# Optimization experiments

Hardware: AMD Instinct MI355X
Metric: run time of the kernel (lower is better)

Reference implementation:

```python
import jax, jax.numpy as jnp
import numpy as np

EPS = 1e-6


def _clinear(xr, xi, wr, wi):
    # nn.Linear applies x @ W.T; complex multiply (xr+i*xi)(Wr+i*Wi)
    r = xr @ wr.T - xi @ wi.T
    im = xi @ wr.T + xr @ wi.T
    return r, im


def setup_inputs() -> dict:
    key = jax.random.key(0)
    ks = jax.random.split(key, 11)
    B, S, D = 16384, 16, 64
    return {
        "z_real": jax.random.normal(ks[0], (B, D), jnp.float32),
        "z_imag": jax.random.normal(ks[1], (B, D), jnp.float32),
        "mem": jax.random.normal(ks[2], (B, S, 2 * D), jnp.float32),
        "ptr": jax.random.uniform(ks[3], (B, S), jnp.float32),
        "ctrl": jax.random.normal(ks[4], (B, 3), jnp.float32),
        "w_q_real": jax.random.normal(ks[5], (D, D), jnp.float32),
        "w_q_imag": jax.random.normal(ks[6], (D, D), jnp.float32),
        "w_k_real": jax.random.normal(ks[7], (D, D), jnp.float32),
        "w_k_imag": jax.random.normal(ks[8], (D, D), jnp.float32),
        "w_v_real": jax.random.normal(ks[9], (D, D), jnp.float32),
        "w_v_imag": jax.random.normal(ks[10], (D, D), jnp.float32),
    }


def reference(z_real, z_imag, mem, ptr, ctrl,
              w_q_real, w_q_imag, w_k_real, w_k_imag, w_v_real, w_v_imag):
    D = z_real.shape[-1]
    scale = D ** (-0.5)

    # differentiable push/pop/stay gates
    g = jax.nn.sigmoid(ctrl)                      # [B, 3]
    total = g.sum(-1, keepdims=True) + EPS
    push = (g[:, 0:1] / total)                    # [B, 1]
    pop = (g[:, 1:2] / total)
    stay = (g[:, 2:3] / total)

    # pointer shifts (torch.roll semantics)
    ptr_up = jnp.roll(ptr, 1, axis=1)
    ptr_down = jnp.roll(ptr, -1, axis=1)
    new_ptr = push * ptr_up + pop * ptr_down + stay * ptr  # [B, S]

    # blended write of current state into every memory slot
    z_flat = jnp.concatenate([z_real, z_imag], axis=-1)    # [B, 2D]
    p = push[:, :, None]                                   # [B, 1, 1]
    mem_new = mem * (1.0 - p) + p * z_flat[:, None, :]     # [B, S, 2D]

    mr, mi = mem_new[..., :D], mem_new[..., D:]

    # complex attention over memory slots
    qr, qi = _clinear(mr, mi, w_q_real, w_q_imag)
    kr, ki = _clinear(mr, mi, w_k_real, w_k_imag)
    vr, vi = _clinear(mr, mi, w_v_real, w_v_imag)
    q_flat = jnp.concatenate([qr, qi], axis=-1)            # [B, S, 2D]
    k_flat = jnp.concatenate([kr, ki], axis=-1)
    scores = jnp.einsum('bsd,btd->bst', q_flat, k_flat) * scale
    attn = jax.nn.softmax(scores, axis=-1)                 # [B, S, S]
    ar = jnp.einsum('bst,btd->bsd', attn, vr)
    ai = jnp.einsum('bst,btd->bsd', attn, vi)
    attended_flat = jnp.concatenate([ar, ai], axis=-1)     # [B, S, 2D]

    # pointer-weighted read
    read_flat = (attended_flat * new_ptr[:, :, None]).sum(1)  # [B, 2D]
    z_read_real = read_flat[:, :D]
    z_read_imag = read_flat[:, D:]

    active_slots = (new_ptr > 0.1).astype(jnp.float32).sum(1).mean()
    return z_read_real, z_read_imag, mem_new, new_ptr, active_slots
```

## Files before the change

kernel.cpp:

```cpp
#include <hip/hip_runtime.h>
#include <math.h>

#define GRID  256
#define BLK   512
#define NB    8
#define NITER 8

typedef __attribute__((ext_vector_type(8))) short short8;
typedef __attribute__((ext_vector_type(4))) float f32x4;

__device__ __forceinline__ float sigf(float x) { return 1.0f / (1.0f + expf(-x)); }

__device__ __forceinline__ unsigned short f2bf(float x) {
    unsigned u = __float_as_uint(x);
    return (unsigned short)((u + 0x7fffu + ((u >> 16) & 1u)) >> 16);
}
__device__ __forceinline__ float bf2f(unsigned short h) {
    return __uint_as_float(((unsigned)h) << 16);
}

__device__ __forceinline__ void split8(const float4 p0, const float4 p1,
                                       short8& hi, short8& lo) {
    float xs[8] = {p0.x, p0.y, p0.z, p0.w, p1.x, p1.y, p1.z, p1.w};
#pragma unroll
    for (int i = 0; i < 8; ++i) {
        unsigned short h = f2bf(xs[i]);
        hi[i] = (short)h;
        lo[i] = (short)f2bf(xs[i] - bf2f(h));
    }
}

__device__ __forceinline__ float Mmat(const float* __restrict__ wr,
                                      const float* __restrict__ wi, int k, int j) {
    if (j < 64) return (k < 64) ? wr[j * 64 + k] : -wi[j * 64 + (k - 64)];
    return (k < 64) ? wi[(j - 64) * 64 + k] : wr[(j - 64) * 64 + (k - 64)];
}

__global__ void prep_kernel(const float* __restrict__ wqr, const float* __restrict__ wqi,
                            const float* __restrict__ wkr, const float* __restrict__ wki,
                            const float* __restrict__ wvr, const float* __restrict__ wvi,
                            float* __restrict__ G, float* __restrict__ Mv,
                            int* __restrict__ cnt) {
    const int a = blockIdx.x;
    const int bb = threadIdx.x;
    if (a == 0 && bb == 0) *cnt = 0;
    float acc = 0.f;
    for (int j = 0; j < 128; ++j)
        acc += Mmat(wqr, wqi, a, j) * Mmat(wkr, wki, bb, j);
    G[a * 128 + bb] = 0.125f * acc;
    Mv[a * 128 + bb] = Mmat(wvr, wvi, a, bb);
}

__global__ void prep_frag(const float* __restrict__ G, const float* __restrict__ Mv,
                          unsigned short* __restrict__ Gf, unsigned short* __restrict__ Mvf) {
    const int bid = blockIdx.x;
    const int lane = threadIdx.x;
    const int mat = bid >> 5, jt = (bid >> 2) & 7, t = bid & 3;
    const float* X = mat ? Mv : G;
    unsigned short* O = mat ? Mvf : Gf;
    const int quad = lane >> 4, col = lane & 15;
    const int obase = ((jt * 4 + t) * 2) * 512 + lane * 8;
#pragma unroll
    for (int i = 0; i < 8; ++i) {
        int k = t * 32 + quad * 8 + i;
        int j = jt * 16 + col;
        float x = X[k * 128 + j];
        unsigned short h = f2bf(x);
        O[obase + i] = h;
        O[obase + 512 + i] = f2bf(x - bf2f(h));
    }
}

__global__ __launch_bounds__(BLK, 2) void crsn_main(
    const float* __restrict__ z_real, const float* __restrict__ z_imag,
    const float* __restrict__ mem, const float* __restrict__ ptr,
    const float* __restrict__ ctrl,
    const unsigned short* __restrict__ Gf, const unsigned short* __restrict__ Mvf,
    float* __restrict__ o_zr, float* __restrict__ o_zi,
    float* __restrict__ o_mem, float* __restrict__ o_np,
    int* __restrict__ g_cnt) {
    __shared__ __align__(16) float buf[16896];
    __shared__ __align__(16) unsigned short mfrag[33280];
    __shared__ float npl[NB][16];
    __shared__ float wl[NB][16];
    __shared__ float pushl[NB], popl[NB], stayl[NB];
    __shared__ int cnt_lds;

    const int tid = threadIdx.x;
    const int w = tid >> 6;
    const int lane = tid & 63;
    const int quad = lane >> 4;
    const int col = lane & 15;

    if (tid == 0) cnt_lds = 0;

    f32x4 acc1[NB], acc2[NB];

    for (int it = 0; it < NITER; ++it) {
        const int base = blockIdx.x * (NB * NITER) + it * NB;

        if (tid < NB) {
            int b = base + tid;
            float g0 = sigf(ctrl[b * 3 + 0]);
            float g1 = sigf(ctrl[b * 3 + 1]);
            float g2 = sigf(ctrl[b * 3 + 2]);
            float tot = g0 + g1 + g2 + 1e-6f;
            pushl[tid] = g0 / tot; popl[tid] = g1 / tot; stayl[tid] = g2 / tot;
        }

        {
            const float* gsrc = mem + (size_t)base * 2048 + w * 2048;
#pragma unroll
            for (int c = 0; c < 8; ++c) {
                __builtin_amdgcn_global_load_lds(
                    (const __attribute__((address_space(1))) unsigned int*)(gsrc + c * 256 + lane * 4),
                    (__attribute__((address_space(3))) unsigned int*)(&buf[w * 2048 + c * 256]),
                    16, 0, 0);
            }
        }
        __syncthreads();

#pragma unroll
        for (int r = 0; r < 8; ++r) {
            int f = tid + BLK * r;
            int nb = f >> 9, rem = f & 511, su = rem >> 5, kq = rem & 31, k = kq << 2;
            int b = base + nb;
            float p = pushl[nb], q = 1.0f - p;
            float4 m4 = *(const float4*)&buf[nb * 2048 + su * 128 + k];
            float4 z4 = (k < 64) ? *(const float4*)(z_real + (b << 6) + k)
                                 : *(const float4*)(z_imag + (b << 6) + k - 64);
            float4 mn;
            mn.x = m4.x * q + p * z4.x;
            mn.y = m4.y * q + p * z4.y;
            mn.z = m4.z * q + p * z4.z;
            mn.w = m4.w * q + p * z4.w;
            *(float4*)(o_mem + (size_t)b * 2048 + su * 128 + k) = mn;
            int t = k >> 5, q2 = (k >> 3) & 3, i0 = k & 7;
            int bidx = ((nb * 4 + t) * 2) * 520 + (q2 * 16 + su) * 8 + i0;
            ushort4 hv;
            hv.x = f2bf(mn.x); hv.y = f2bf(mn.y); hv.z = f2bf(mn.z); hv.w = f2bf(mn.w);
            ushort4 lv;
            lv.x = f2bf(mn.x - bf2f(hv.x));
            lv.y = f2bf(mn.y - bf2f(hv.y));
            lv.z = f2bf(mn.z - bf2f(hv.z));
            lv.w = f2bf(mn.w - bf2f(hv.w));
            *(ushort4*)&mfrag[bidx] = hv;
            *(ushort4*)&mfrag[bidx + 520] = lv;
        }
        __syncthreads();

        {
#pragma unroll
            for (int nb = 0; nb < NB; ++nb) {
                acc1[nb] = (f32x4){0.f, 0.f, 0.f, 0.f};
                acc2[nb] = (f32x4){0.f, 0.f, 0.f, 0.f};
            }
#pragma unroll
            for (int t = 0; t < 4; ++t) {
                const int fb = ((w * 4 + t) * 2) * 512 + lane * 8;
                short8 Gh = *(const short8*)(Gf + fb);
                short8 Gl = *(const short8*)(Gf + fb + 512);
                short8 Mh = *(const short8*)(Mvf + fb);
                short8 Ml = *(const short8*)(Mvf + fb + 512);
#pragma unroll
                for (int nb = 0; nb < NB; ++nb) {
                    const unsigned short* mp = &mfrag[((nb * 4 + t) * 2) * 520 + lane * 8];
                    short8 ah = *(const short8*)mp;
                    short8 al = *(const short8*)(mp + 520);
                    acc1[nb] = __builtin_amdgcn_mfma_f32_16x16x32_bf16(ah, Gh, acc1[nb], 0, 0, 0);
                    acc1[nb] = __builtin_amdgcn_mfma_f32_16x16x32_bf16(ah, Gl, acc1[nb], 0, 0, 0);
                    acc1[nb] = __builtin_amdgcn_mfma_f32_16x16x32_bf16(al, Gh, acc1[nb], 0, 0, 0);
                    acc2[nb] = __builtin_amdgcn_mfma_f32_16x16x32_bf16(ah, Mh, acc2[nb], 0, 0, 0);
                    acc2[nb] = __builtin_amdgcn_mfma_f32_16x16x32_bf16(ah, Ml, acc2[nb], 0, 0, 0);
                    acc2[nb] = __builtin_amdgcn_mfma_f32_16x16x32_bf16(al, Mh, acc2[nb], 0, 0, 0);
                }
            }
#pragma unroll
            for (int nb = 0; nb < NB; ++nb) {
#pragma unroll
                for (int reg = 0; reg < 4; ++reg)
                    buf[nb * 2112 + (quad * 4 + reg) * 132 + w * 16 + col] = acc1[nb][reg];
            }
        }
        __syncthreads();

        {
            const int b2 = base + w;
            float npv = 0.f;
            if (lane < 16) {
                float pv = ptr[(b2 << 4) + lane];
                float up = ptr[(b2 << 4) + ((lane + 15) & 15)];
                float dn = ptr[(b2 << 4) + ((lane + 1) & 15)];
                npv = pushl[w] * up + popl[w] * dn + stayl[w] * pv;
                o_np[(b2 << 4) + lane] = npv;
                npl[w][lane] = npv;
            }
            unsigned long long bal = __ballot(npv > 0.1f);
            if (lane == 0) atomicAdd(&cnt_lds, (int)__popcll(bal));

            f32x4 sc = (f32x4){0.f, 0.f, 0.f, 0.f};
#pragma unroll
            for (int t = 0; t < 4; ++t) {
                const float* tp = &buf[w * 2112 + col * 132 + t * 32 + quad * 8];
                float4 p0 = *(const float4*)tp;
                float4 p1 = *(const float4*)(tp + 4);
                short8 ah, al;
                split8(p0, p1, ah, al);
                const unsigned short* mp = &mfrag[((w * 4 + t) * 2) * 520 + lane * 8];
                short8 bh = *(const short8*)mp;
                short8 bl = *(const short8*)(mp + 520);
                sc = __builtin_amdgcn_mfma_f32_16x16x32_bf16(ah, bh, sc, 0, 0, 0);
                sc = __builtin_amdgcn_mfma_f32_16x16x32_bf16(ah, bl, sc, 0, 0, 0);
                sc = __builtin_amdgcn_mfma_f32_16x16x32_bf16(al, bh, sc, 0, 0, 0);
            }
            float at[4];
#pragma unroll
            for (int reg = 0; reg < 4; ++reg) {
                float v = sc[reg];
                float mx = v;
                mx = fmaxf(mx, __shfl_xor(mx, 1));
                mx = fmaxf(mx, __shfl_xor(mx, 2));
                mx = fmaxf(mx, __shfl_xor(mx, 4));
                mx = fmaxf(mx, __shfl_xor(mx, 8));
                float e = expf(v - mx);
                float s2 = e;
                s2 += __shfl_xor(s2, 1);
                s2 += __shfl_xor(s2, 2);
                s2 += __shfl_xor(s2, 4);
                s2 += __shfl_xor(s2, 8);
                at[reg] = e / s2;
            }
            float wv = npl[w][quad * 4 + 0] * at[0] + npl[w][quad * 4 + 1] * at[1]
                     + npl[w][quad * 4 + 2] * at[2] + npl[w][quad * 4 + 3] * at[3];
            wv += __shfl_xor(wv, 16);
            wv += __shfl_xor(wv, 32);
            if (lane < 16) wl[w][lane] = wv;
        }
        __syncthreads();

#pragma unroll
        for (int nb = 0; nb < NB; ++nb) {
            float pr = wl[nb][quad * 4 + 0] * acc2[nb][0]
                     + wl[nb][quad * 4 + 1] * acc2[nb][1]
                     + wl[nb][quad * 4 + 2] * acc2[nb][2]
                     + wl[nb][quad * 4 + 3] * acc2[nb][3];
            pr += __shfl_xor(pr, 16);
            pr += __shfl_xor(pr, 32);
            if (lane < 16) {
                int j = w * 16 + lane;
                int b2 = base + nb;
                if (j < 64) o_zr[(b2 << 6) + j] = pr;
                else        o_zi[(b2 << 6) + j - 64] = pr;
            }
        }
    }
    __syncthreads();
    if (tid == 0) atomicAdd(g_cnt, cnt_lds);
}

__global__ void fin_kernel(const int* __restrict__ cnt, float* __restrict__ o_act) {
    *o_act = (float)(*cnt) / 16384.0f;
}

extern "C" void kernel_launch(void* const* d_in, const int* in_sizes, int n_in,
                              void* d_out, int out_size, void* d_ws, size_t ws_size,
                              hipStream_t stream) {
    const float* z_real = (const float*)d_in[0];
    const float* z_imag = (const float*)d_in[1];
    const float* mem    = (const float*)d_in[2];
    const float* ptr    = (const float*)d_in[3];
    const float* ctrl   = (const float*)d_in[4];
    const float* wqr = (const float*)d_in[5];
    const float* wqi = (const float*)d_in[6];
    const float* wkr = (const float*)d_in[7];
    const float* wki = (const float*)d_in[8];
    const float* wvr = (const float*)d_in[9];
    const float* wvi = (const float*)d_in[10];

    float* out = (float*)d_out;
    float* o_zr  = out;
    float* o_zi  = out + 16384 * 64;
    float* o_mem = out + 2 * 16384 * 64;
    float* o_np  = o_mem + 16384 * 16 * 128;
    float* o_act = o_np + 16384 * 16;

    int*   cnt = (int*)d_ws;
    float* G   = (float*)((char*)d_ws + 256);
    float* Mv  = G + 128 * 128;
    unsigned short* Gfr  = (unsigned short*)(Mv + 128 * 128);
    unsigned short* Mvfr = Gfr + 32768;

    hipLaunchKernelGGL(prep_kernel, dim3(128), dim3(128), 0, stream,
                       wqr, wqi, wkr, wki, wvr, wvi, G, Mv, cnt);
    hipLaunchKernelGGL(prep_frag, dim3(64), dim3(64), 0, stream, G, Mv, Gfr, Mvfr);
    hipLaunchKernelGGL(crsn_main, dim3(GRID), dim3(BLK), 0, stream,
                       z_real, z_imag, mem, ptr, ctrl, Gfr, Mvfr,
                       o_zr, o_zi, o_mem, o_np, cnt);
    hipLaunchKernelGGL(fin_kernel, dim3(1), dim3(1), 0, stream, cnt, o_act);
}
```

Baseline: 375.8 us.

## Halve batch per block, double grid, drop a barrier, and truncate lo-bf16 splits

Each block now handles 4 batch elements per iteration instead of 8, and the grid doubles to 512 blocks. Shared memory shrinks and launch bounds rise to 4 blocks per CU, aimed at higher occupancy and better latency hiding. Each wave pair loads and blends one batch element itself and waits on its own loads with s_waitcnt, removing the first __syncthreads. Gate values are recomputed per wave rather than shared through LDS, and the pointer values are broadcast with shuffles. The low-part bf16 conversion now truncates instead of rounding, saving ALU work at a small accuracy cost. Only half the waves do the attention stage, so that phase has less parallelism per block.

```diff
diff --git a/kernel.cpp b/kernel.cpp
--- a/kernel.cpp
+++ b/kernel.cpp
@@ -1,9 +1,9 @@
 #include <hip/hip_runtime.h>
 #include <math.h>
 
-#define GRID  256
+#define GRID  512
 #define BLK   512
-#define NB    8
+#define NB    4
 #define NITER 8
 
 typedef __attribute__((ext_vector_type(8))) short short8;
@@ -18,6 +18,9 @@
 __device__ __forceinline__ float bf2f(unsigned short h) {
     return __uint_as_float(((unsigned)h) << 16);
 }
+__device__ __forceinline__ unsigned short f2bf_trunc(float x) {
+    return (unsigned short)(__float_as_uint(x) >> 16);
+}
 
 __device__ __forceinline__ void split8(const float4 p0, const float4 p1,
                                        short8& hi, short8& lo) {
@@ -26,7 +29,7 @@
     for (int i = 0; i < 8; ++i) {
         unsigned short h = f2bf(xs[i]);
         hi[i] = (short)h;
-        lo[i] = (short)f2bf(xs[i] - bf2f(h));
+        lo[i] = (short)f2bf_trunc(xs[i] - bf2f(h));
     }
 }
 
@@ -67,11 +70,11 @@
         float x = X[k * 128 + j];
         unsigned short h = f2bf(x);
         O[obase + i] = h;
-        O[obase + 512 + i] = f2bf(x - bf2f(h));
+        O[obase + 512 + i] = f2bf_trunc(x - bf2f(h));
     }
 }
 
-__global__ __launch_bounds__(BLK, 2) void crsn_main(
+__global__ __launch_bounds__(BLK, 4) void crsn_main(
     const float* __restrict__ z_real, const float* __restrict__ z_imag,
     const float* __restrict__ mem, const float* __restrict__ ptr,
     const float* __restrict__ ctrl,
@@ -79,11 +82,9 @@
     float* __restrict__ o_zr, float* __restrict__ o_zi,
     float* __restrict__ o_mem, float* __restrict__ o_np,
     int* __restrict__ g_cnt) {
-    __shared__ __align__(16) float buf[16896];
-    __shared__ __align__(16) unsigned short mfrag[33280];
-    __shared__ float npl[NB][16];
+    __shared__ __align__(16) float buf[NB * 2112];
+    __shared__ __align__(16) unsigned short mfrag[NB * 8 * 520];
     __shared__ float wl[NB][16];
-    __shared__ float pushl[NB], popl[NB], stayl[NB];
     __shared__ int cnt_lds;
 
     const int tid = threadIdx.x;
@@ -91,6 +92,8 @@
     const int lane = tid & 63;
     const int quad = lane >> 4;
     const int col = lane & 15;
+    const int snb = w >> 1;
+    const int half = w & 1;
 
     if (tid == 0) cnt_lds = 0;
 
@@ -98,52 +101,47 @@
 
     for (int it = 0; it < NITER; ++it) {
         const int base = blockIdx.x * (NB * NITER) + it * NB;
-
-        if (tid < NB) {
-            int b = base + tid;
-            float g0 = sigf(ctrl[b * 3 + 0]);
-            float g1 = sigf(ctrl[b * 3 + 1]);
-            float g2 = sigf(ctrl[b * 3 + 2]);
-            float tot = g0 + g1 + g2 + 1e-6f;
-            pushl[tid] = g0 / tot; popl[tid] = g1 / tot; stayl[tid] = g2 / tot;
-        }
+        const int bs = base + snb;
 
         {
-            const float* gsrc = mem + (size_t)base * 2048 + w * 2048;
-#pragma unroll
-            for (int c = 0; c < 8; ++c) {
+            const float* gsrc = mem + (size_t)bs * 2048 + half * 1024;
+#pragma unroll
+            for (int c = 0; c < 4; ++c) {
                 __builtin_amdgcn_global_load_lds(
                     (const __attribute__((address_space(1))) unsigned int*)(gsrc + c * 256 + lane * 4),
-                    (__attribute__((address_space(3))) unsigned int*)(&buf[w * 2048 + c * 256]),
+                    (__attribute__((address_space(3))) unsigned int*)(&buf[snb * 2112 + half * 1024 + c * 256]),
                     16, 0, 0);
             }
         }
-        __syncthreads();
-
-#pragma unroll
-        for (int r = 0; r < 8; ++r) {
-            int f = tid + BLK * r;
-            int nb = f >> 9, rem = f & 511, su = rem >> 5, kq = rem & 31, k = kq << 2;
-            int b = base + nb;
-            float p = pushl[nb], q = 1.0f - p;
-            float4 m4 = *(const float4*)&buf[nb * 2048 + su * 128 + k];
-            float4 z4 = (k < 64) ? *(const float4*)(z_real + (b << 6) + k)
-                                 : *(const float4*)(z_imag + (b << 6) + k - 64);
+        float g0 = sigf(ctrl[bs * 3 + 0]);
+        float g1 = sigf(ctrl[bs * 3 + 1]);
+        float g2 = sigf(ctrl[bs * 3 + 2]);
+        float push = g0 / (g0 + g1 + g2 + 1e-6f);
+        float qq = 1.0f - push;
+
+        __builtin_amdgcn_s_waitcnt(0x0f70);
+
+#pragma unroll
+        for (int c = 0; c < 4; ++c) {
+            int fi = half * 256 + c * 64 + lane;
+            int su = fi >> 5, k = (fi & 31) << 2;
+            float4 m4 = *(const float4*)&buf[snb * 2112 + fi * 4];
+            float4 z4 = (k < 64) ? *(const float4*)(z_real + (bs << 6) + k)
+                                 : *(const float4*)(z_imag + (bs << 6) + k - 64);
             float4 mn;
-            mn.x = m4.x * q + p * z4.x;
-            mn.y = m4.y * q + p * z4.y;
-            mn.z = m4.z * q + p * z4.z;
-            mn.w = m4.w * q + p * z4.w;
-            *(float4*)(o_mem + (size_t)b * 2048 + su * 128 + k) = mn;
+            mn.x = m4.x * qq + push * z4.x;
+            mn.y = m4.y * qq + push * z4.y;
+            mn.z = m4.z * qq + push * z4.z;
+            mn.w = m4.w * qq + push * z4.w;
+            *(float4*)(o_mem + (size_t)bs * 2048 + fi * 4) = mn;
             int t = k >> 5, q2 = (k >> 3) & 3, i0 = k & 7;
-            int bidx = ((nb * 4 + t) * 2) * 520 + (q2 * 16 + su) * 8 + i0;
-            ushort4 hv;
+            int bidx = ((snb * 4 + t) * 2) * 520 + (q2 * 16 + su) * 8 + i0;
+            ushort4 hv, lv;
             hv.x = f2bf(mn.x); hv.y = f2bf(mn.y); hv.z = f2bf(mn.z); hv.w = f2bf(mn.w);
-            ushort4 lv;
-            lv.x = f2bf(mn.x - bf2f(hv.x));
-            lv.y = f2bf(mn.y - bf2f(hv.y));
-            lv.z = f2bf(mn.z - bf2f(hv.z));
-            lv.w = f2bf(mn.w - bf2f(hv.w));
+            lv.x = f2bf_trunc(mn.x - bf2f(hv.x));
+            lv.y = f2bf_trunc(mn.y - bf2f(hv.y));
+            lv.z = f2bf_trunc(mn.z - bf2f(hv.z));
+            lv.w = f2bf_trunc(mn.w - bf2f(hv.w));
             *(ushort4*)&mfrag[bidx] = hv;
             *(ushort4*)&mfrag[bidx + 520] = lv;
         }
@@ -157,11 +155,12 @@
             }
 #pragma unroll
             for (int t = 0; t < 4; ++t) {
-                const int fb = ((w * 4 + t) * 2) * 512 + lane * 8;
-                short8 Gh = *(const short8*)(Gf + fb);
-                short8 Gl = *(const short8*)(Gf + fb + 512);
-                short8 Mh = *(const short8*)(Mvf + fb);
-                short8 Ml = *(const short8*)(Mvf + fb + 512);
+                const unsigned short* fb = Gf + ((w * 4 + t) * 2) * 512 + lane * 8;
+                const unsigned short* fb2 = Mvf + ((w * 4 + t) * 2) * 512 + lane * 8;
+                short8 Gh = *(const short8*)fb;
+                short8 Gl = *(const short8*)(fb + 512);
+                short8 Mh = *(const short8*)fb2;
+                short8 Ml = *(const short8*)(fb2 + 512);
 #pragma unroll
                 for (int nb = 0; nb < NB; ++nb) {
                     const unsigned short* mp = &mfrag[((nb * 4 + t) * 2) * 520 + lane * 8];
@@ -176,26 +175,28 @@
                 }
             }
 #pragma unroll
-            for (int nb = 0; nb < NB; ++nb) {
+            for (int nb = 0; nb < NB; ++nb)
 #pragma unroll
                 for (int reg = 0; reg < 4; ++reg)
                     buf[nb * 2112 + (quad * 4 + reg) * 132 + w * 16 + col] = acc1[nb][reg];
-            }
         }
         __syncthreads();
 
-        {
+        if (w < NB) {
             const int b2 = base + w;
-            float npv = 0.f;
-            if (lane < 16) {
-                float pv = ptr[(b2 << 4) + lane];
-                float up = ptr[(b2 << 4) + ((lane + 15) & 15)];
-                float dn = ptr[(b2 << 4) + ((lane + 1) & 15)];
-                npv = pushl[w] * up + popl[w] * dn + stayl[w] * pv;
-                o_np[(b2 << 4) + lane] = npv;
-                npl[w][lane] = npv;
-            }
-            unsigned long long bal = __ballot(npv > 0.1f);
+            float h0 = sigf(ctrl[b2 * 3 + 0]);
+            float h1 = sigf(ctrl[b2 * 3 + 1]);
+            float h2 = sigf(ctrl[b2 * 3 + 2]);
+            float ht = h0 + h1 + h2 + 1e-6f;
+            float pushb = h0 / ht, popb = h1 / ht, stayb = h2 / ht;
+
+            int s = lane & 15;
+            float pv = ptr[(b2 << 4) + s];
+            float up = ptr[(b2 << 4) + ((s + 15) & 15)];
+            float dn = ptr[(b2 << 4) + ((s + 1) & 15)];
+            float npv = pushb * up + popb * dn + stayb * pv;
+            if (lane < 16) o_np[(b2 << 4) + lane] = npv;
+            unsigned long long bal = __ballot(lane < 16 && npv > 0.1f);
             if (lane == 0) atomicAdd(&cnt_lds, (int)__popcll(bal));
 
             f32x4 sc = (f32x4){0.f, 0.f, 0.f, 0.f};
@@ -230,8 +231,8 @@
                 s2 += __shfl_xor(s2, 8);
                 at[reg] = e / s2;
             }
-            float wv = npl[w][quad * 4 + 0] * at[0] + npl[w][quad * 4 + 1] * at[1]
-                     + npl[w][quad * 4 + 2] * at[2] + npl[w][quad * 4 + 3] * at[3];
+            float wv = __shfl(npv, quad * 4 + 0) * at[0] + __shfl(npv, quad * 4 + 1) * at[1]
+                     + __shfl(npv, quad * 4 + 2) * at[2] + __shfl(npv, quad * 4 + 3) * at[3];
             wv += __shfl_xor(wv, 16);
             wv += __shfl_xor(wv, 32);
             if (lane < 16) wl[w][lane] = wv;
@@ -247,7 +248,7 @@
             pr += __shfl_xor(pr, 16);
             pr += __shfl_xor(pr, 32);
             if (lane < 16) {
-                int j = w * 16 + lane;
+                int j = (w << 4) + lane;
                 int b2 = base + nb;
                 if (j < 64) o_zr[(b2 << 6) + j] = pr;
                 else        o_zi[(b2 << 6) + j - 64] = pr;
```

After: 373.1 us. Within noise of the previous version (-0.7%).
